# Performance work log

Measured on AMD Instinct MI355X. Metric: run time of the kernel, lower is better.

Reference implementation:

```python
import jax, jax.numpy as jnp
import numpy as np

D_MODEL = 1024
H = 16
D_K = D_MODEL // H


def setup_inputs() -> dict:
    key = jax.random.key(0)
    ks = jax.random.split(key, 12)
    B, S = 2, 2048
    scale = 1.0 / np.sqrt(D_MODEL)
    inp = {
        "q": jax.random.normal(ks[0], (B, S, D_MODEL), jnp.float32),
        "k": jax.random.normal(ks[1], (B, S, D_MODEL), jnp.float32),
        "v": jax.random.normal(ks[2], (B, S, D_MODEL), jnp.float32),
        "mask": jnp.ones((B, 1, S, S), jnp.int32),
        # nn.Linear weights are [out, in]; applied as x @ W.T + b
        "Wq": jax.random.normal(ks[3], (D_MODEL, D_MODEL), jnp.float32) * scale,
        "bq": jnp.zeros((D_MODEL,), jnp.float32),
        "Wk": jax.random.normal(ks[4], (D_MODEL, D_MODEL), jnp.float32) * scale,
        "bk": jnp.zeros((D_MODEL,), jnp.float32),
        "Wv": jax.random.normal(ks[5], (D_MODEL, D_MODEL), jnp.float32) * scale,
        "bv": jnp.zeros((D_MODEL,), jnp.float32),
        "Wo": jax.random.normal(ks[6], (D_MODEL, D_MODEL), jnp.float32) * scale,
        "bo": jnp.zeros((D_MODEL,), jnp.float32),
    }
    return inp


def reference(q, k, v, mask, Wq, bq, Wk, bk, Wv, bv, Wo, bo):
    B, S, _ = q.shape
    # projections
    query = q @ Wq.T + bq
    key_ = k @ Wk.T + bk
    value = v @ Wv.T + bv
    # [B, S, D] -> [B, H, S, d_k]
    query = query.reshape(B, S, H, D_K).transpose(0, 2, 1, 3)
    key_ = key_.reshape(B, S, H, D_K).transpose(0, 2, 1, 3)
    value = value.reshape(B, S, H, D_K).transpose(0, 2, 1, 3)
    # scaled dot-product attention with full [B,H,S,S] scores (as in source)
    scores = jnp.einsum("bhqd,bhkd->bhqk", query, key_) / jnp.sqrt(
        jnp.asarray(D_K, query.dtype)
    )
    # NOTE: source uses masked_fill value = -1e-09 (faithful reproduction)
    scores = jnp.where(mask == 0, jnp.asarray(-1e-09, scores.dtype), scores)
    attn = jax.nn.softmax(scores, axis=-1)
    # dropout p=0.0 -> identity
    x = jnp.einsum("bhqk,bhkd->bhqd", attn, value)
    x = x.transpose(0, 2, 1, 3).reshape(B, S, H * D_K)
    return x @ Wo.T + bo
```

## Files before the change

### kernel.cpp

```cpp
#include <hip/hip_runtime.h>
#include <hip/hip_bf16.h>
#include <stdint.h>

#define DI __device__ __forceinline__

typedef __bf16 bf16x8 __attribute__((ext_vector_type(8)));
typedef __bf16 bf16x4 __attribute__((ext_vector_type(4)));
typedef float  f32x4  __attribute__((ext_vector_type(4)));

constexpr int Bc = 2, Sc = 2048, Dm = 1024, Hc = 16;
constexpr int Mrows = Bc * Sc;
constexpr float LOG2E = 1.4426950408889634f;

DI void async16(void* lds, const void* g) {
  __builtin_amdgcn_global_load_lds(
      (const __attribute__((address_space(1))) void*)g,
      (__attribute__((address_space(3))) void*)lds, 16, 0, 0);
}

DI void cvt_one(const float* __restrict__ in, __bf16* __restrict__ out, int i) {
  const f32x4* in4 = (const f32x4*)in;
  f32x4 a = in4[2 * i], b = in4[2 * i + 1];
  bf16x8 o;
#pragma unroll
  for (int j = 0; j < 4; ++j) { o[j] = (__bf16)a[j]; o[4 + j] = (__bf16)b[j]; }
  ((bf16x8*)out)[i] = o;
}

__global__ void cvt3(const float* __restrict__ a, const float* __restrict__ b,
                     const float* __restrict__ c, __bf16* __restrict__ oa,
                     __bf16* __restrict__ ob, __bf16* __restrict__ oc, int n8) {
  int i = blockIdx.x * blockDim.x + threadIdx.x;
  if (i >= n8) return;
  cvt_one(a, oa, i); cvt_one(b, ob, i); cvt_one(c, oc, i);
}

__global__ void cvt4(const float* __restrict__ a, const float* __restrict__ b,
                     const float* __restrict__ c, const float* __restrict__ d,
                     __bf16* __restrict__ oa, __bf16* __restrict__ ob,
                     __bf16* __restrict__ oc, __bf16* __restrict__ od, int n8) {
  int i = blockIdx.x * blockDim.x + threadIdx.x;
  if (i >= n8) return;
  cvt_one(a, oa, i); cvt_one(b, ob, i); cvt_one(c, oc, i); cvt_one(d, od, i);
}

__global__ void pack_mask(const int* __restrict__ m, unsigned long long* __restrict__ bits) {
  const int total = Bc * Sc * Sc;
  const int nth = gridDim.x * blockDim.x;
  for (int i = blockIdx.x * blockDim.x + threadIdx.x; i < total; i += nth) {
    unsigned long long b = __ballot(m[i] != 0);
    if ((threadIdx.x & 63) == 0) bits[i >> 6] = b;
  }
}

DI void gemm_core(const __bf16* __restrict__ A, const __bf16* __restrict__ Bw,
                  __bf16* As, __bf16* Bs, int m0, int n0, int t, f32x4 (&acc)[4][4]) {
  const int lane = t & 63, wv = t >> 6;
  const int lo = lane & 15, hi = lane >> 4;
  const int wm = (wv >> 1) * 64, wn = (wv & 1) * 64;
  const int rowA = t >> 2, kc8 = (t & 3) * 8;

  for (int k0 = 0; k0 < 1024; k0 += 32) {
    __syncthreads();
    async16(&As[t * 8],        A  + (size_t)(m0 + rowA) * 1024      + k0 + kc8);
    async16(&As[t * 8 + 2048], A  + (size_t)(m0 + rowA + 64) * 1024 + k0 + kc8);
    async16(&Bs[t * 8],        Bw + (size_t)(n0 + rowA) * 1024      + k0 + kc8);
    async16(&Bs[t * 8 + 2048], Bw + (size_t)(n0 + rowA + 64) * 1024 + k0 + kc8);
    __syncthreads();
    bf16x8 af[4], bfr[4];
#pragma unroll
    for (int i = 0; i < 4; ++i)
      af[i] = *(const bf16x8*)&As[(wm + i * 16 + lo) * 32 + hi * 8];
#pragma unroll
    for (int j = 0; j < 4; ++j)
      bfr[j] = *(const bf16x8*)&Bs[(wn + j * 16 + lo) * 32 + hi * 8];
#pragma unroll
    for (int i = 0; i < 4; ++i)
#pragma unroll
      for (int j = 0; j < 4; ++j)
        acc[i][j] = __builtin_amdgcn_mfma_f32_16x16x32_bf16(af[i], bfr[j], acc[i][j], 0, 0, 0);
  }
}

__global__ __launch_bounds__(256)
void gemm_qkv(const __bf16* __restrict__ Aq, const __bf16* __restrict__ Ak,
              const __bf16* __restrict__ Av, const __bf16* __restrict__ Wqb,
              const __bf16* __restrict__ Wkb, const __bf16* __restrict__ Wvb,
              const float* __restrict__ bq, const float* __restrict__ bk,
              const float* __restrict__ bv,
              __bf16* __restrict__ Qh, __bf16* __restrict__ Kh, __bf16* __restrict__ Vt) {
  __shared__ __bf16 As[128 * 32];
  __shared__ __bf16 Bs[128 * 32];
  const int which = blockIdx.x >> 8;
  int local = blockIdx.x & 255;
  local = (local & 7) * 32 + (local >> 3);
  const int m0 = (local >> 3) * 128, n0 = (local & 7) * 128;
  const __bf16* A    = which == 0 ? Aq  : which == 1 ? Ak  : Av;
  const __bf16* Bw   = which == 0 ? Wqb : which == 1 ? Wkb : Wvb;
  const float*  bias = which == 0 ? bq  : which == 1 ? bk  : bv;
  const int t = threadIdx.x;

  f32x4 acc[4][4] = {};
  gemm_core(A, Bw, As, Bs, m0, n0, t, acc);

  const int lane = t & 63, wv = t >> 6, lo = lane & 15, hi = lane >> 4;
  const int wm = (wv >> 1) * 64, wn = (wv & 1) * 64;

  if (which < 2) {
    __bf16* C = which ? Kh : Qh;
#pragma unroll
    for (int mi = 0; mi < 4; ++mi) {
      const int mbase = m0 + wm + mi * 16 + hi * 4;
      const int b = mbase >> 11, s = mbase & 2047;
#pragma unroll
      for (int ni = 0; ni < 4; ++ni) {
        const int n = n0 + wn + ni * 16 + lo;
        const int h = n >> 6, d = n & 63;
        const float bb = bias[n];
        __bf16* p = C + ((size_t)(b * Hc + h) * Sc + s) * 64 + d;
#pragma unroll
        for (int r = 0; r < 4; ++r)
          p[(size_t)r * 64] = (__bf16)(acc[mi][ni][r] + bb);
      }
    }
  } else {
#pragma unroll
    for (int mi = 0; mi < 4; ++mi) {
      const int mbase = m0 + wm + mi * 16 + hi * 4;
      const int b = mbase >> 11, s0 = mbase & 2047;
#pragma unroll
      for (int ni = 0; ni < 4; ++ni) {
        const int n = n0 + wn + ni * 16 + lo;
        const int h = n >> 6, d = n & 63;
        const float bb = bias[n];
        bf16x4 pk;
#pragma unroll
        for (int r = 0; r < 4; ++r) pk[r] = (__bf16)(acc[mi][ni][r] + bb);
        *(bf16x4*)(Vt + ((size_t)(b * Hc + h) * 64 + d) * Sc + s0) = pk;
      }
    }
  }
}

__global__ __launch_bounds__(256)
void gemm_o(const __bf16* __restrict__ A, const __bf16* __restrict__ Bw,
            const float* __restrict__ bias, float* __restrict__ C) {
  __shared__ __bf16 As[128 * 32];
  __shared__ __bf16 Bs[128 * 32];
  int bid = blockIdx.x;
  bid = (bid & 7) * 32 + (bid >> 3);
  const int m0 = (bid >> 3) * 128, n0 = (bid & 7) * 128;
  const int t = threadIdx.x;

  f32x4 acc[4][4] = {};
  gemm_core(A, Bw, As, Bs, m0, n0, t, acc);

  const int lane = t & 63, wv = t >> 6, lo = lane & 15, hi = lane >> 4;
  const int wm = (wv >> 1) * 64, wn = (wv & 1) * 64;
#pragma unroll
  for (int mi = 0; mi < 4; ++mi) {
    const int mbase = m0 + wm + mi * 16 + hi * 4;
#pragma unroll
    for (int ni = 0; ni < 4; ++ni) {
      const int n = n0 + wn + ni * 16 + lo;
      const float bb = bias[n];
#pragma unroll
      for (int r = 0; r < 4; ++r)
        C[(size_t)(mbase + r) * 1024 + n] = acc[mi][ni][r] + bb;
    }
  }
}

__global__ __launch_bounds__(256)
void attn_fwd(const __bf16* __restrict__ Qh, const __bf16* __restrict__ Kh,
              const __bf16* __restrict__ Vt, const unsigned long long* __restrict__ mbits,
              __bf16* __restrict__ X) {
  __shared__ __bf16 Ks[2][64 * 64];
  __shared__ __bf16 Vs[2][64 * 64];
  __shared__ __bf16 Pq[4][2][16][80];

  int bid = blockIdx.x;
  bid = (bid & 7) * 64 + (bid >> 3);
  const int qblk = bid & 15, h = (bid >> 4) & 15, b = bid >> 8;
  const int t = threadIdx.x, lane = t & 63, wv = t >> 6;
  const int lo = lane & 15, hi = lane >> 4;
  const int q0 = qblk * 128 + wv * 32;

  const size_t headoff = (size_t)(b * Hc + h) * Sc * 64;
  const __bf16* Qp = Qh + headoff + (size_t)q0 * 64;
  const __bf16* Kp = Kh + headoff;
  const __bf16* Vp = Vt + headoff;

  bf16x8 qf[2][2];
#pragma unroll
  for (int qt = 0; qt < 2; ++qt)
#pragma unroll
    for (int c = 0; c < 2; ++c)
      qf[qt][c] = *(const bf16x8*)&Qp[(qt * 16 + lo) * 64 + c * 32 + hi * 8];

  f32x4 o[2][4] = {};
  float mr[2] = {-1e30f, -1e30f}, lr[2] = {0.f, 0.f};

  const int srow = t >> 3, scb = t & 7;
  const int ksrc = ((scb ^ (srow & 7)) * 8);

  auto stage = [&](int buf, int kb) {
    async16(&Ks[buf][t * 8],        Kp + (size_t)(kb + srow) * 64 + ksrc);
    async16(&Ks[buf][t * 8 + 2048], Kp + (size_t)(kb + srow + 32) * 64 + ksrc);
    async16(&Vs[buf][t * 8],        Vp + (size_t)srow * Sc + kb + ksrc);
    async16(&Vs[buf][t * 8 + 2048], Vp + (size_t)(srow + 32) * Sc + kb + ksrc);
  };

  stage(0, 0);
  int cur = 0;
  const int xr = (lo & 7) << 3;

  for (int kb = 0; kb < Sc; kb += 64) {
    __syncthreads();
    if (kb + 64 < Sc) stage(cur ^ 1, kb + 64);

    bf16x8 kf[4][2];
#pragma unroll
    for (int kc = 0; kc < 4; ++kc)
#pragma unroll
      for (int c = 0; c < 2; ++c)
        kf[kc][c] = *(const bf16x8*)&Ks[cur][(kc * 16 + lo) * 64 + ((c * 32 + hi * 8) ^ xr)];

#pragma unroll
    for (int qt = 0; qt < 2; ++qt) {
      f32x4 sc[4];
#pragma unroll
      for (int kc = 0; kc < 4; ++kc) {
        f32x4 z = {0.f, 0.f, 0.f, 0.f};
        sc[kc] = __builtin_amdgcn_mfma_f32_16x16x32_bf16(kf[kc][0], qf[qt][0], z, 0, 0, 0);
        sc[kc] = __builtin_amdgcn_mfma_f32_16x16x32_bf16(kf[kc][1], qf[qt][1], sc[kc], 0, 0, 0);
      }
      const unsigned long long mb =
          mbits[(size_t)(b * Sc + q0 + qt * 16 + lo) * (Sc / 64) + (kb >> 6)];
      const bool allm = __all(mb == ~0ull);
      float pvv[4][4];
#pragma unroll
      for (int kc = 0; kc < 4; ++kc)
#pragma unroll
        for (int r = 0; r < 4; ++r) pvv[kc][r] = sc[kc][r] * 0.125f;
      if (!allm) {
#pragma unroll
        for (int kc = 0; kc < 4; ++kc)
#pragma unroll
          for (int r = 0; r < 4; ++r)
            if (!((mb >> (kc * 16 + hi * 4 + r)) & 1ull)) pvv[kc][r] = -1e-9f;
      }
      float pmax = -1e30f;
#pragma unroll
      for (int kc = 0; kc < 4; ++kc)
#pragma unroll
        for (int r = 0; r < 4; ++r) pmax = fmaxf(pmax, pvv[kc][r]);
      pmax = fmaxf(pmax, __shfl_xor(pmax, 16));
      pmax = fmaxf(pmax, __shfl_xor(pmax, 32));

      float m = mr[qt];
      if (!__all(pmax <= m + 8.f)) {
        const float mn = fmaxf(m, pmax);
        const float fs = exp2f((m - mn) * LOG2E);
        lr[qt] *= fs;
#pragma unroll
        for (int d0 = 0; d0 < 4; ++d0) o[qt][d0] *= fs;
        m = mn; mr[qt] = mn;
      }
      const float mj = m * LOG2E;
      float rs = 0.f;
#pragma unroll
      for (int kc = 0; kc < 4; ++kc)
#pragma unroll
        for (int r = 0; r < 4; ++r) {
          const float p = exp2f(__builtin_fmaf(pvv[kc][r], LOG2E, -mj));
          pvv[kc][r] = p; rs += p;
        }
      rs += __shfl_xor(rs, 16);
      rs += __shfl_xor(rs, 32);
      lr[qt] += rs;
#pragma unroll
      for (int kc = 0; kc < 4; ++kc) {
        bf16x4 pk;
#pragma unroll
        for (int r = 0; r < 4; ++r) pk[r] = (__bf16)pvv[kc][r];
        *(bf16x4*)&Pq[wv][qt][lo][kc * 16 + hi * 4] = pk;
      }
    }

    bf16x8 vf[4][2];
#pragma unroll
    for (int d0 = 0; d0 < 4; ++d0)
#pragma unroll
      for (int c = 0; c < 2; ++c)
        vf[d0][c] = *(const bf16x8*)&Vs[cur][(d0 * 16 + lo) * 64 + ((c * 32 + hi * 8) ^ xr)];
#pragma unroll
    for (int qt = 0; qt < 2; ++qt) {
      bf16x8 pa[2];
#pragma unroll
      for (int c = 0; c < 2; ++c)
        pa[c] = *(const bf16x8*)&Pq[wv][qt][lo][c * 32 + hi * 8];
#pragma unroll
      for (int d0 = 0; d0 < 4; ++d0) {
        o[qt][d0] = __builtin_amdgcn_mfma_f32_16x16x32_bf16(vf[d0][0], pa[0], o[qt][d0], 0, 0, 0);
        o[qt][d0] = __builtin_amdgcn_mfma_f32_16x16x32_bf16(vf[d0][1], pa[1], o[qt][d0], 0, 0, 0);
      }
    }
    cur ^= 1;
  }

#pragma unroll
  for (int qt = 0; qt < 2; ++qt) {
    const float inv = 1.f / lr[qt];
#pragma unroll
    for (int d0 = 0; d0 < 4; ++d0) {
      bf16x4 st;
#pragma unroll
      for (int r = 0; r < 4; ++r) st[r] = (__bf16)(o[qt][d0][r] * inv);
      *(bf16x4*)&X[(size_t)(b * Sc + q0 + qt * 16 + lo) * 1024 + h * 64 + d0 * 16 + hi * 4] = st;
    }
  }
}

extern "C" void kernel_launch(void* const* d_in, const int* in_sizes, int n_in,
                              void* d_out, int out_size, void* d_ws, size_t ws_size,
                              hipStream_t stream) {
  const float* q  = (const float*)d_in[0];
  const float* k  = (const float*)d_in[1];
  const float* v  = (const float*)d_in[2];
  const int*   mask = (const int*)d_in[3];
  const float* Wq = (const float*)d_in[4];
  const float* bq = (const float*)d_in[5];
  const float* Wk = (const float*)d_in[6];
  const float* bk = (const float*)d_in[7];
  const float* Wv = (const float*)d_in[8];
  const float* bv = (const float*)d_in[9];
  const float* Wo = (const float*)d_in[10];
  const float* bo = (const float*)d_in[11];

  const size_t MB = 1u << 20;
  if (ws_size < 66 * MB) return;

  char* ws = (char*)d_ws;
  __bf16* wqb  = (__bf16*)(ws + 0 * MB);
  __bf16* wkb  = (__bf16*)(ws + 2 * MB);
  __bf16* wvb  = (__bf16*)(ws + 4 * MB);
  __bf16* wob  = (__bf16*)(ws + 6 * MB);
  __bf16* qbin = (__bf16*)(ws + 8 * MB);
  __bf16* kbin = (__bf16*)(ws + 16 * MB);
  __bf16* vbin = (__bf16*)(ws + 24 * MB);
  __bf16* Qh   = (__bf16*)(ws + 32 * MB);
  __bf16* Kh   = (__bf16*)(ws + 40 * MB);
  __bf16* Vt   = (__bf16*)(ws + 48 * MB);
  __bf16* Xat  = (__bf16*)(ws + 56 * MB);
  unsigned long long* mbits = (unsigned long long*)(ws + 64 * MB);

  const int nIn8 = Mrows * Dm / 8;
  const int nW8  = Dm * Dm / 8;
  cvt3<<<nIn8 / 256, 256, 0, stream>>>(q, k, v, qbin, kbin, vbin, nIn8);
  cvt4<<<nW8 / 256, 256, 0, stream>>>(Wq, Wk, Wv, Wo, wqb, wkb, wvb, wob, nW8);
  pack_mask<<<4096, 256, 0, stream>>>(mask, mbits);

  gemm_qkv<<<768, 256, 0, stream>>>(qbin, kbin, vbin, wqb, wkb, wvb, bq, bk, bv, Qh, Kh, Vt);

  attn_fwd<<<512, 256, 0, stream>>>(Qh, Kh, Vt, mbits, Xat);

  gemm_o<<<256, 256, 0, stream>>>(Xat, wob, bo, (float*)d_out);
}
```

Measured before the change: 310.5 us.

## Double-buffer GEMM LDS tiles and split attention across eight waves per block

The GEMM core now double-buffers its A/B LDS tiles, prefetching the next k-slice while computing the current one, and drops to one barrier per iteration. The attention kernel moves to 512 threads, with each wave owning 16 query rows instead of 32, and K/V staging is spread across more threads. MFMA sections are wrapped in s_setprio. This aims to hide global-load latency and raise occupancy and latency hiding, at the cost of twice the LDS per GEMM block and less K/V register reuse per wave in attention.

```diff
diff --git a/kernel.cpp b/kernel.cpp
--- a/kernel.cpp
+++ b/kernel.cpp
@@ -60,37 +60,48 @@
   const int wm = (wv >> 1) * 64, wn = (wv & 1) * 64;
   const int rowA = t >> 2, kc8 = (t & 3) * 8;
 
+  auto stage = [&](int buf, int k0) {
+    __bf16* as = As + buf * 4096;
+    __bf16* bs = Bs + buf * 4096;
+    async16(&as[t * 8],        A  + (size_t)(m0 + rowA) * 1024      + k0 + kc8);
+    async16(&as[t * 8 + 2048], A  + (size_t)(m0 + rowA + 64) * 1024 + k0 + kc8);
+    async16(&bs[t * 8],        Bw + (size_t)(n0 + rowA) * 1024      + k0 + kc8);
+    async16(&bs[t * 8 + 2048], Bw + (size_t)(n0 + rowA + 64) * 1024 + k0 + kc8);
+  };
+
+  stage(0, 0);
+  __syncthreads();
+  int cur = 0;
   for (int k0 = 0; k0 < 1024; k0 += 32) {
-    __syncthreads();
-    async16(&As[t * 8],        A  + (size_t)(m0 + rowA) * 1024      + k0 + kc8);
-    async16(&As[t * 8 + 2048], A  + (size_t)(m0 + rowA + 64) * 1024 + k0 + kc8);
-    async16(&Bs[t * 8],        Bw + (size_t)(n0 + rowA) * 1024      + k0 + kc8);
-    async16(&Bs[t * 8 + 2048], Bw + (size_t)(n0 + rowA + 64) * 1024 + k0 + kc8);
-    __syncthreads();
+    if (k0 + 32 < 1024) stage(cur ^ 1, k0 + 32);
+    const __bf16* as = As + cur * 4096;
+    const __bf16* bs = Bs + cur * 4096;
     bf16x8 af[4], bfr[4];
 #pragma unroll
     for (int i = 0; i < 4; ++i)
-      af[i] = *(const bf16x8*)&As[(wm + i * 16 + lo) * 32 + hi * 8];
+      af[i] = *(const bf16x8*)&as[(wm + i * 16 + lo) * 32 + hi * 8];
 #pragma unroll
     for (int j = 0; j < 4; ++j)
-      bfr[j] = *(const bf16x8*)&Bs[(wn + j * 16 + lo) * 32 + hi * 8];
+      bfr[j] = *(const bf16x8*)&bs[(wn + j * 16 + lo) * 32 + hi * 8];
 #pragma unroll
     for (int i = 0; i < 4; ++i)
 #pragma unroll
       for (int j = 0; j < 4; ++j)
         acc[i][j] = __builtin_amdgcn_mfma_f32_16x16x32_bf16(af[i], bfr[j], acc[i][j], 0, 0, 0);
-  }
-}
-
-__global__ __launch_bounds__(256)
+    __syncthreads();
+    cur ^= 1;
+  }
+}
+
+__global__ __launch_bounds__(256, 3)
 void gemm_qkv(const __bf16* __restrict__ Aq, const __bf16* __restrict__ Ak,
               const __bf16* __restrict__ Av, const __bf16* __restrict__ Wqb,
               const __bf16* __restrict__ Wkb, const __bf16* __restrict__ Wvb,
               const float* __restrict__ bq, const float* __restrict__ bk,
               const float* __restrict__ bv,
               __bf16* __restrict__ Qh, __bf16* __restrict__ Kh, __bf16* __restrict__ Vt) {
-  __shared__ __bf16 As[128 * 32];
-  __shared__ __bf16 Bs[128 * 32];
+  __shared__ __bf16 As[2][128 * 32];
+  __shared__ __bf16 Bs[2][128 * 32];
   const int which = blockIdx.x >> 8;
   int local = blockIdx.x & 255;
   local = (local & 7) * 32 + (local >> 3);
@@ -101,7 +112,7 @@
   const int t = threadIdx.x;
 
   f32x4 acc[4][4] = {};
-  gemm_core(A, Bw, As, Bs, m0, n0, t, acc);
+  gemm_core(A, Bw, &As[0][0], &Bs[0][0], m0, n0, t, acc);
 
   const int lane = t & 63, wv = t >> 6, lo = lane & 15, hi = lane >> 4;
   const int wm = (wv >> 1) * 64, wn = (wv & 1) * 64;
@@ -142,18 +153,18 @@
   }
 }
 
-__global__ __launch_bounds__(256)
+__global__ __launch_bounds__(256, 3)
 void gemm_o(const __bf16* __restrict__ A, const __bf16* __restrict__ Bw,
             const float* __restrict__ bias, float* __restrict__ C) {
-  __shared__ __bf16 As[128 * 32];
-  __shared__ __bf16 Bs[128 * 32];
+  __shared__ __bf16 As[2][128 * 32];
+  __shared__ __bf16 Bs[2][128 * 32];
   int bid = blockIdx.x;
   bid = (bid & 7) * 32 + (bid >> 3);
   const int m0 = (bid >> 3) * 128, n0 = (bid & 7) * 128;
   const int t = threadIdx.x;
 
   f32x4 acc[4][4] = {};
-  gemm_core(A, Bw, As, Bs, m0, n0, t, acc);
+  gemm_core(A, Bw, &As[0][0], &Bs[0][0], m0, n0, t, acc);
 
   const int lane = t & 63, wv = t >> 6, lo = lane & 15, hi = lane >> 4;
   const int wm = (wv >> 1) * 64, wn = (wv & 1) * 64;
@@ -171,154 +182,137 @@
   }
 }
 
-__global__ __launch_bounds__(256)
+__global__ __launch_bounds__(512, 4)
 void attn_fwd(const __bf16* __restrict__ Qh, const __bf16* __restrict__ Kh,
               const __bf16* __restrict__ Vt, const unsigned long long* __restrict__ mbits,
               __bf16* __restrict__ X) {
   __shared__ __bf16 Ks[2][64 * 64];
   __shared__ __bf16 Vs[2][64 * 64];
-  __shared__ __bf16 Pq[4][2][16][80];
+  __shared__ __bf16 Pq[8][16][72];
 
   int bid = blockIdx.x;
   bid = (bid & 7) * 64 + (bid >> 3);
   const int qblk = bid & 15, h = (bid >> 4) & 15, b = bid >> 8;
   const int t = threadIdx.x, lane = t & 63, wv = t >> 6;
   const int lo = lane & 15, hi = lane >> 4;
-  const int q0 = qblk * 128 + wv * 32;
+  const int q0 = qblk * 128 + wv * 16;
 
   const size_t headoff = (size_t)(b * Hc + h) * Sc * 64;
   const __bf16* Qp = Qh + headoff + (size_t)q0 * 64;
   const __bf16* Kp = Kh + headoff;
   const __bf16* Vp = Vt + headoff;
 
-  bf16x8 qf[2][2];
-#pragma unroll
-  for (int qt = 0; qt < 2; ++qt)
-#pragma unroll
-    for (int c = 0; c < 2; ++c)
-      qf[qt][c] = *(const bf16x8*)&Qp[(qt * 16 + lo) * 64 + c * 32 + hi * 8];
-
-  f32x4 o[2][4] = {};
-  float mr[2] = {-1e30f, -1e30f}, lr[2] = {0.f, 0.f};
+  bf16x8 qf[2];
+#pragma unroll
+  for (int c = 0; c < 2; ++c)
+    qf[c] = *(const bf16x8*)&Qp[lo * 64 + c * 32 + hi * 8];
+
+  f32x4 o[4] = {};
+  float mr = -1e30f, lr = 0.f;
 
   const int srow = t >> 3, scb = t & 7;
   const int ksrc = ((scb ^ (srow & 7)) * 8);
 
   auto stage = [&](int buf, int kb) {
-    async16(&Ks[buf][t * 8],        Kp + (size_t)(kb + srow) * 64 + ksrc);
-    async16(&Ks[buf][t * 8 + 2048], Kp + (size_t)(kb + srow + 32) * 64 + ksrc);
-    async16(&Vs[buf][t * 8],        Vp + (size_t)srow * Sc + kb + ksrc);
-    async16(&Vs[buf][t * 8 + 2048], Vp + (size_t)(srow + 32) * Sc + kb + ksrc);
+    async16(&Ks[buf][t * 8], Kp + (size_t)(kb + srow) * 64 + ksrc);
+    async16(&Vs[buf][t * 8], Vp + (size_t)srow * Sc + kb + ksrc);
   };
 
   stage(0, 0);
   int cur = 0;
   const int xr = (lo & 7) << 3;
+  const unsigned long long* mrow = mbits + (size_t)(b * Sc + q0 + lo) * (Sc / 64);
 
   for (int kb = 0; kb < Sc; kb += 64) {
     __syncthreads();
     if (kb + 64 < Sc) stage(cur ^ 1, kb + 64);
 
-    bf16x8 kf[4][2];
+    f32x4 sc[4];
+    __builtin_amdgcn_s_setprio(1);
+#pragma unroll
+    for (int kc = 0; kc < 4; ++kc) {
+      bf16x8 kf0 = *(const bf16x8*)&Ks[cur][(kc * 16 + lo) * 64 + ((hi * 8) ^ xr)];
+      bf16x8 kf1 = *(const bf16x8*)&Ks[cur][(kc * 16 + lo) * 64 + ((32 + hi * 8) ^ xr)];
+      f32x4 z = {0.f, 0.f, 0.f, 0.f};
+      sc[kc] = __builtin_amdgcn_mfma_f32_16x16x32_bf16(kf0, qf[0], z, 0, 0, 0);
+      sc[kc] = __builtin_amdgcn_mfma_f32_16x16x32_bf16(kf1, qf[1], sc[kc], 0, 0, 0);
+    }
+    __builtin_amdgcn_s_setprio(0);
+
+    const unsigned long long mb = mrow[kb >> 6];
+    const bool allm = __all(mb == ~0ull);
+    float pvv[4][4];
 #pragma unroll
     for (int kc = 0; kc < 4; ++kc)
 #pragma unroll
-      for (int c = 0; c < 2; ++c)
-        kf[kc][c] = *(const bf16x8*)&Ks[cur][(kc * 16 + lo) * 64 + ((c * 32 + hi * 8) ^ xr)];
-
-#pragma unroll
-    for (int qt = 0; qt < 2; ++qt) {
-      f32x4 sc[4];
-#pragma unroll
-      for (int kc = 0; kc < 4; ++kc) {
-        f32x4 z = {0.f, 0.f, 0.f, 0.f};
-        sc[kc] = __builtin_amdgcn_mfma_f32_16x16x32_bf16(kf[kc][0], qf[qt][0], z, 0, 0, 0);
-        sc[kc] = __builtin_amdgcn_mfma_f32_16x16x32_bf16(kf[kc][1], qf[qt][1], sc[kc], 0, 0, 0);
+      for (int r = 0; r < 4; ++r) pvv[kc][r] = sc[kc][r] * 0.125f;
+    if (!allm) {
+#pragma unroll
+      for (int kc = 0; kc < 4; ++kc)
+#pragma unroll
+        for (int r = 0; r < 4; ++r)
+          if (!((mb >> (kc * 16 + hi * 4 + r)) & 1ull)) pvv[kc][r] = -1e-9f;
+    }
+    float pmax = -1e30f;
+#pragma unroll
+    for (int kc = 0; kc < 4; ++kc)
+#pragma unroll
+      for (int r = 0; r < 4; ++r) pmax = fmaxf(pmax, pvv[kc][r]);
+    pmax = fmaxf(pmax, __shfl_xor(pmax, 16));
+    pmax = fmaxf(pmax, __shfl_xor(pmax, 32));
+
+    if (!__all(pmax <= mr + 8.f)) {
+      const float mn = fmaxf(mr, pmax);
+      const float fs = exp2f((mr - mn) * LOG2E);
+      lr *= fs;
+#pragma unroll
+      for (int d0 = 0; d0 < 4; ++d0) o[d0] *= fs;
+      mr = mn;
+    }
+    const float mj = mr * LOG2E;
+    float rs = 0.f;
+#pragma unroll
+    for (int kc = 0; kc < 4; ++kc)
+#pragma unroll
+      for (int r = 0; r < 4; ++r) {
+        const float p = exp2f(__builtin_fmaf(pvv[kc][r], LOG2E, -mj));
+        pvv[kc][r] = p; rs += p;
       }
-      const unsigned long long mb =
-          mbits[(size_t)(b * Sc + q0 + qt * 16 + lo) * (Sc / 64) + (kb >> 6)];
-      const bool allm = __all(mb == ~0ull);
-      float pvv[4][4];
-#pragma unroll
-      for (int kc = 0; kc < 4; ++kc)
-#pragma unroll
-        for (int r = 0; r < 4; ++r) pvv[kc][r] = sc[kc][r] * 0.125f;
-      if (!allm) {
-#pragma unroll
-        for (int kc = 0; kc < 4; ++kc)
-#pragma unroll
-          for (int r = 0; r < 4; ++r)
-            if (!((mb >> (kc * 16 + hi * 4 + r)) & 1ull)) pvv[kc][r] = -1e-9f;
-      }
-      float pmax = -1e30f;
-#pragma unroll
-      for (int kc = 0; kc < 4; ++kc)
-#pragma unroll
-        for (int r = 0; r < 4; ++r) pmax = fmaxf(pmax, pvv[kc][r]);
-      pmax = fmaxf(pmax, __shfl_xor(pmax, 16));
-      pmax = fmaxf(pmax, __shfl_xor(pmax, 32));
-
-      float m = mr[qt];
-      if (!__all(pmax <= m + 8.f)) {
-        const float mn = fmaxf(m, pmax);
-        const float fs = exp2f((m - mn) * LOG2E);
-        lr[qt] *= fs;
-#pragma unroll
-        for (int d0 = 0; d0 < 4; ++d0) o[qt][d0] *= fs;
-        m = mn; mr[qt] = mn;
-      }
-      const float mj = m * LOG2E;
-      float rs = 0.f;
-#pragma unroll
-      for (int kc = 0; kc < 4; ++kc)
-#pragma unroll
-        for (int r = 0; r < 4; ++r) {
-          const float p = exp2f(__builtin_fmaf(pvv[kc][r], LOG2E, -mj));
-          pvv[kc][r] = p; rs += p;
-        }
-      rs += __shfl_xor(rs, 16);
-      rs += __shfl_xor(rs, 32);
-      lr[qt] += rs;
-#pragma unroll
-      for (int kc = 0; kc < 4; ++kc) {
-        bf16x4 pk;
-#pragma unroll
-        for (int r = 0; r < 4; ++r) pk[r] = (__bf16)pvv[kc][r];
-        *(bf16x4*)&Pq[wv][qt][lo][kc * 16 + hi * 4] = pk;
-      }
-    }
-
-    bf16x8 vf[4][2];
-#pragma unroll
-    for (int d0 = 0; d0 < 4; ++d0)
-#pragma unroll
-      for (int c = 0; c < 2; ++c)
-        vf[d0][c] = *(const bf16x8*)&Vs[cur][(d0 * 16 + lo) * 64 + ((c * 32 + hi * 8) ^ xr)];
-#pragma unroll
-    for (int qt = 0; qt < 2; ++qt) {
-      bf16x8 pa[2];
-#pragma unroll
-      for (int c = 0; c < 2; ++c)
-        pa[c] = *(const bf16x8*)&Pq[wv][qt][lo][c * 32 + hi * 8];
-#pragma unroll
-      for (int d0 = 0; d0 < 4; ++d0) {
-        o[qt][d0] = __builtin_amdgcn_mfma_f32_16x16x32_bf16(vf[d0][0], pa[0], o[qt][d0], 0, 0, 0);
-        o[qt][d0] = __builtin_amdgcn_mfma_f32_16x16x32_bf16(vf[d0][1], pa[1], o[qt][d0], 0, 0, 0);
-      }
-    }
+    rs += __shfl_xor(rs, 16);
+    rs += __shfl_xor(rs, 32);
+    lr += rs;
+
+#pragma unroll
+    for (int kc = 0; kc < 4; ++kc) {
+      bf16x4 pk;
+#pragma unroll
+      for (int r = 0; r < 4; ++r) pk[r] = (__bf16)pvv[kc][r];
+      *(bf16x4*)&Pq[wv][lo][kc * 16 + hi * 4] = pk;
+    }
+
+    bf16x8 pa[2];
+#pragma unroll
+    for (int c = 0; c < 2; ++c)
+      pa[c] = *(const bf16x8*)&Pq[wv][lo][c * 32 + hi * 8];
+    __builtin_amdgcn_s_setprio(1);
+#pragma unroll
+    for (int d0 = 0; d0 < 4; ++d0) {
+      bf16x8 vf0 = *(const bf16x8*)&Vs[cur][(d0 * 16 + lo) * 64 + ((hi * 8) ^ xr)];
+      bf16x8 vf1 = *(const bf16x8*)&Vs[cur][(d0 * 16 + lo) * 64 + ((32 + hi * 8) ^ xr)];
+      o[d0] = __builtin_amdgcn_mfma_f32_16x16x32_bf16(vf0, pa[0], o[d0], 0, 0, 0);
+      o[d0] = __builtin_amdgcn_mfma_f32_16x16x32_bf16(vf1, pa[1], o[d0], 0, 0, 0);
+    }
+    __builtin_amdgcn_s_setprio(0);
     cur ^= 1;
   }
 
-#pragma unroll
-  for (int qt = 0; qt < 2; ++qt) {
-    const float inv = 1.f / lr[qt];
-#pragma unroll
-    for (int d0 = 0; d0 < 4; ++d0) {
-      bf16x4 st;
-#pragma unroll
-      for (int r = 0; r < 4; ++r) st[r] = (__bf16)(o[qt][d0][r] * inv);
-      *(bf16x4*)&X[(size_t)(b * Sc + q0 + qt * 16 + lo) * 1024 + h * 64 + d0 * 16 + hi * 4] = st;
-    }
+  const float inv = 1.f / lr;
+#pragma unroll
+  for (int d0 = 0; d0 < 4; ++d0) {
+    bf16x4 st;
+#pragma unroll
+    for (int r = 0; r < 4; ++r) st[r] = (__bf16)(o[d0][r] * inv);
+    *(bf16x4*)&X[(size_t)(b * Sc + q0 + lo) * 1024 + h * 64 + d0 * 16 + hi * 4] = st;
   }
 }
 
@@ -363,7 +357,7 @@
 
   gemm_qkv<<<768, 256, 0, stream>>>(qbin, kbin, vbin, wqb, wkb, wvb, bq, bk, bv, Qh, Kh, Vt);
 
-  attn_fwd<<<512, 256, 0, stream>>>(Qh, Kh, Vt, mbits, Xat);
+  attn_fwd<<<512, 512, 0, stream>>>(Qh, Kh, Vt, mbits, Xat);
 
   gemm_o<<<256, 256, 0, stream>>>(Xat, wob, bo, (float*)d_out);
 }
```

Result: faster. 284.5 us (-8.4%).
